# Performance work log

Hardware: AMD Instinct MI355X
Metric: run time of the kernel (lower is better)

## Reference

```python
import jax, jax.numpy as jnp
import numpy as np

STAGE = (20, 20, 20)  # stage spatial size taken from prediction.raw_displacement.shape[2:]


def setup_inputs() -> dict:
    key = jax.random.key(0)
    k1, k2, k3 = jax.random.split(key, 3)
    B, C = 2, 16
    N = STAGE[0] * STAGE[1] * STAGE[2]
    canonical_source = jax.random.normal(k1, (B, C, 64, 64, 64), jnp.float32)
    canonical_target = jax.random.normal(k2, (B, C, 64, 64, 64), jnp.float32)
    # predicted positions live in voxel coordinates of the stage grid
    expected_target_positions = jax.random.uniform(k3, (B, N, 3), jnp.float32) * (STAGE[0] - 1)
    return {
        "canonical_source": canonical_source,
        "canonical_target": canonical_target,
        "expected_target_positions": expected_target_positions,
    }


def reference(canonical_source, canonical_target, expected_target_positions):
    B, C = canonical_source.shape[:2]
    D, H, W = STAGE
    N = D * H * W

    # F.interpolate(mode='trilinear', align_corners=False) == jax.image.resize half-pixel linear
    rs = jax.image.resize(canonical_source, (B, C, D, H, W), method='trilinear')
    rt = jax.image.resize(canonical_target, (B, C, D, H, W), method='trilinear')

    s = rs.reshape(B, C, N).transpose(0, 2, 1)  # (B, N, C)
    t = rt.reshape(B, C, N).transpose(0, 2, 1)  # (B, N, C)

    # squared Euclidean pairwise distances (argmin identical to cdist argmin)
    d2 = (jnp.sum(s * s, axis=-1)[:, :, None]
          - 2.0 * jnp.einsum('bnc,bmc->bnm', s, t)
          + jnp.sum(t * t, axis=-1)[:, None, :])  # (B, N, N)
    nearest = jnp.argmin(d2, axis=-1)  # (B, N)

    dt = canonical_source.dtype
    grid = jnp.stack(
        jnp.meshgrid(jnp.arange(D, dtype=dt), jnp.arange(H, dtype=dt),
                     jnp.arange(W, dtype=dt), indexing='ij'),
        axis=-1).reshape(N, 3)  # (N, 3) voxel coords of target grid

    gathered_target = grid[nearest]  # (B, N, 3)
    return jnp.mean(jnp.abs(expected_target_positions - gathered_target))
```

## Files before the change

kernel.cpp:

```cpp
#include <hip/hip_runtime.h>
#include <stdint.h>
#include <math.h>

#define BDIM   2
#define CDIM   16
#define INS    64
#define OUTS   20
#define NPTS   8000
#define TOTN   (BDIM*NPTS)

using f64x4 = __attribute__((ext_vector_type(4))) double;

#define MFMA64(a, b, c) __builtin_amdgcn_mfma_f64_16x16x4f64((a), (b), (c), 0, 0, 0)


__global__ __launch_bounds__(256) void k_resize(const float* __restrict__ src,
                                                const float* __restrict__ tgt,
                                                double* __restrict__ sfeat2,
                                                double* __restrict__ tfeat) {
    __shared__ double wts[OUTS][8];
    __shared__ int    st[OUTS];
    __shared__ int    cnt[OUTS];
    __shared__ double plane[INS * INS];
    __shared__ double hplane[OUTS * INS];

    int tid = threadIdx.x;
    if (tid < OUTS) {
        double sample = (tid + 0.5) * 3.2 - 0.5;
        int lo = (int)ceil(sample - 3.2);
        int hi = (int)floor(sample + 3.2);
        if (lo < 0) lo = 0;
        if (hi > INS - 1) hi = INS - 1;
        int c = hi - lo + 1;
        double w[8];
        double sum = 0.0;
        for (int k = 0; k < 8; ++k) {
            double ww = 0.0;
            if (k < c) {
                double x = fabs(sample - (double)(lo + k)) * (1.0 / 3.2);
                ww = (x < 1.0) ? (1.0 - x) : 0.0;
            }
            w[k] = ww; sum += ww;
        }
        for (int k = 0; k < 8; ++k) wts[tid][k] = w[k] / sum;
        st[tid] = lo; cnt[tid] = c;
    }
    __syncthreads();

    int od  = blockIdx.x;
    int c   = blockIdx.y;
    int sb  = blockIdx.z;
    int sel = sb >> 1;
    int b   = sb & 1;

    const float* in = (sel ? tgt : src) + (((size_t)(b * CDIM + c)) << 18);

    int sd = st[od], cd = cnt[od];
    double acc[16];
#pragma unroll
    for (int i = 0; i < 16; ++i) acc[i] = 0.0;
    for (int t = 0; t < cd; ++t) {
        double wd = wts[od][t];
        const float* p = in + (((size_t)(sd + t)) << 12) + tid;
#pragma unroll
        for (int i = 0; i < 16; ++i)
            acc[i] = fma(wd, (double)p[i << 8], acc[i]);
    }
#pragma unroll
    for (int i = 0; i < 16; ++i) plane[tid + (i << 8)] = acc[i];
    __syncthreads();

    for (int e = tid; e < OUTS * INS; e += 256) {
        int oh = e >> 6, w = e & 63;
        int sh = st[oh], ch = cnt[oh];
        double a = 0.0;
        for (int t = 0; t < ch; ++t)
            a = fma(wts[oh][t], plane[((sh + t) << 6) + w], a);
        hplane[e] = a;
    }
    __syncthreads();

    double* outf = sel ? tfeat : sfeat2;
    for (int e = tid; e < OUTS * OUTS; e += 256) {
        int oh = e / OUTS, ow = e - oh * OUTS;
        int sw = st[ow], cw = cnt[ow];
        const double* hp = &hplane[(oh << 6) + sw];
        double a = 0.0;
        for (int t = 0; t < cw; ++t)
            a = fma(wts[ow][t], hp[t], a);
        if (sel == 0) a = -2.0 * a;
        int n = (od * OUTS + oh) * OUTS + ow;
        outf[((size_t)(b * NPTS + n)) * CDIM + c] = a;
    }
}

__global__ void k_t2(const double* __restrict__ tfeat, double* __restrict__ t2) {
    int i = blockIdx.x * blockDim.x + threadIdx.x;
    if (i >= TOTN) return;
    const double* p = tfeat + (size_t)i * CDIM;
    double a = 0, b = 0, c = 0, d = 0;
#pragma unroll
    for (int k = 0; k < 4; ++k) {
        a = fma(p[4*k+0], p[4*k+0], a);
        b = fma(p[4*k+1], p[4*k+1], b);
        c = fma(p[4*k+2], p[4*k+2], c);
        d = fma(p[4*k+3], p[4*k+3], d);
    }
    t2[i] = (a + b) + (c + d);
}

__global__ __launch_bounds__(256, 2) void k_argmin(const double* __restrict__ sfeat2,
                                                   const double* __restrict__ tfeat,
                                                   const double* __restrict__ t2,
                                                   double* __restrict__ pscore,
                                                   int* __restrict__ pidx,
                                                   int mchunk, int nchunk) {
    int b     = blockIdx.z;
    int chunk = blockIdx.y;
    int lane  = threadIdx.x & 63;
    int wp    = threadIdx.x >> 6;
    int nbase = blockIdx.x << 7;
    int n0    = nbase + (wp << 4);
    int n1    = n0 + 64;
    int lr    = lane & 15;
    int lq    = lane >> 4;

    f64x4 z = {0.0, 0.0, 0.0, 0.0};
    f64x4 calA = MFMA64((double)lr, 0.25, z);
    f64x4 calB = MFMA64(0.25, (double)lr, z);
    int ncol = (int)(calB[0] + 0.5);

    __shared__ int ptab[16];
#pragma unroll
    for (int j = 0; j < 4; ++j) {
        int r = (int)(calA[j] + 0.5);
        ptab[r] = (lq << 2) + j;
    }
    __syncthreads();
    int prow = ptab[lr];

    int nn0 = n0 + lr; if (nn0 > NPTS - 1) nn0 = NPTS - 1;
    int nn1 = n1 + lr; if (nn1 > NPTS - 1) nn1 = NPTS - 1;
    const double* sb0 = sfeat2 + ((size_t)(b * NPTS + nn0)) * CDIM + (lq << 2);
    const double* sb1 = sfeat2 + ((size_t)(b * NPTS + nn1)) * CDIM + (lq << 2);
    double b00 = sb0[0], b01 = sb0[1], b02 = sb0[2], b03 = sb0[3];
    double b10 = sb1[0], b11 = sb1[1], b12 = sb1[2], b13 = sb1[3];

    const double* tb  = tfeat + (size_t)b * NPTS * CDIM;
    const double* t2b = t2 + (size_t)b * NPTS;

    int mbase = chunk * mchunk;
    int iters = mchunk >> 5;

    const double* tA = tb + ((size_t)(mbase + prow)) * CDIM + (lq << 2);
    const double* tV = t2b + mbase + (lq << 2);

    double bs00 = 1e300, bs01 = 1e300, bs10 = 1e300, bs11 = 1e300;
    int    ip00 = 0, ip01 = 0, ip10 = 0, ip11 = 0;
    int    ij00 = 0, ij01 = 0, ij10 = 0, ij11 = 0;

    f64x4 aE0, aE1, vE0, vE1, aO0, aO1, vO0, vO1;

#define LOADP(P, A0, A1, V0, V1)                                   \
    {  const double* pa_ = tA + (size_t)((P) << 5) * CDIM;         \
       A0 = *(const f64x4*)(pa_);                                  \
       A1 = *(const f64x4*)(pa_ + (CDIM << 4));                    \
       const double* pv_ = tV + ((P) << 5);                        \
       V0 = *(const f64x4*)(pv_);                                  \
       V1 = *(const f64x4*)(pv_ + 16); }

#define FOLD(AC, BS, IP, IJ, P)                                    \
    {  double jb_ = AC[0]; int jj_ = 0;                            \
       if (AC[1] < jb_) { jb_ = AC[1]; jj_ = 1; }                  \
       if (AC[2] < jb_) { jb_ = AC[2]; jj_ = 2; }                  \
       if (AC[3] < jb_) { jb_ = AC[3]; jj_ = 3; }                  \
       if (jb_ < BS) { BS = jb_; IP = (P); IJ = jj_; } }

#define BODYP(P, A0, A1, V0, V1)                                   \
    {  f64x4 a00 = V0, a01 = V1, a10 = V0, a11 = V1;               \
       a00 = MFMA64(A0[0], b00, a00);                              \
       a10 = MFMA64(A0[0], b10, a10);                              \
       a01 = MFMA64(A1[0], b00, a01);                              \
       a11 = MFMA64(A1[0], b10, a11);                              \
       a00 = MFMA64(A0[1], b01, a00);                              \
       a10 = MFMA64(A0[1], b11, a10);                              \
       a01 = MFMA64(A1[1], b01, a01);                              \
       a11 = MFMA64(A1[1], b11, a11);                              \
       a00 = MFMA64(A0[2], b02, a00);                              \
       a10 = MFMA64(A0[2], b12, a10);                              \
       a01 = MFMA64(A1[2], b02, a01);                              \
       a11 = MFMA64(A1[2], b12, a11);                              \
       a00 = MFMA64(A0[3], b03, a00);                              \
       a10 = MFMA64(A0[3], b13, a10);                              \
       a01 = MFMA64(A1[3], b03, a01);                              \
       a11 = MFMA64(A1[3], b13, a11);                              \
       FOLD(a00, bs00, ip00, ij00, P)                              \
       FOLD(a01, bs01, ip01, ij01, P)                              \
       FOLD(a10, bs10, ip10, ij10, P)                              \
       FOLD(a11, bs11, ip11, ij11, P) }

    LOADP(0, aE0, aE1, vE0, vE1);
    if (iters > 1) LOADP(1, aO0, aO1, vO0, vO1);

    int p = 0;
    for (; p + 2 < iters; p += 2) {
        BODYP(p, aE0, aE1, vE0, vE1);
        LOADP(p + 2, aE0, aE1, vE0, vE1);
        BODYP(p + 1, aO0, aO1, vO0, vO1);
        if (p + 3 < iters) LOADP(p + 3, aO0, aO1, vO0, vO1);
    }
    BODYP(p, aE0, aE1, vE0, vE1);
    if (p + 1 < iters) BODYP(p + 1, aO0, aO1, vO0, vO1);

#undef LOADP
#undef FOLD
#undef BODYP

    int m00 = mbase + (ip00 << 5) + (lq << 2) + ij00;
    int m01 = mbase + (ip01 << 5) + 16 + (lq << 2) + ij01;
    int m10 = mbase + (ip10 << 5) + (lq << 2) + ij10;
    int m11 = mbase + (ip11 << 5) + 16 + (lq << 2) + ij11;

    double fb0 = bs00; int fm0 = m00;
    if (bs01 < fb0 || (bs01 == fb0 && m01 < fm0)) { fb0 = bs01; fm0 = m01; }
    double fb1 = bs10; int fm1 = m10;
    if (bs11 < fb1 || (bs11 == fb1 && m11 < fm1)) { fb1 = bs11; fm1 = m11; }

#pragma unroll
    for (int off = 16; off <= 32; off <<= 1) {
        double ob = __shfl_xor(fb0, off, 64);
        int    om = __shfl_xor(fm0, off, 64);
        if (ob < fb0 || (ob == fb0 && om < fm0)) { fb0 = ob; fm0 = om; }
        double ob1 = __shfl_xor(fb1, off, 64);
        int    om1 = __shfl_xor(fm1, off, 64);
        if (ob1 < fb1 || (ob1 == fb1 && om1 < fm1)) { fb1 = ob1; fm1 = om1; }
    }
    if (lq == 0) {
        size_t base = ((size_t)(b * nchunk + chunk)) * NPTS;
        int ns0 = n0 + ncol;
        pscore[base + ns0] = fb0;
        pidx[base + ns0]   = fm0;
        int ns1 = n1 + ncol;
        if (ns1 < NPTS) {
            pscore[base + ns1] = fb1;
            pidx[base + ns1]   = fm1;
        }
    }
}

__global__ void k_mergeloss(const double* __restrict__ pscore,
                            const int* __restrict__ pidx,
                            const float* __restrict__ expd,
                            double* __restrict__ lpart, int nchunk) {
    int gid = blockIdx.x * 256 + threadIdx.x;
    double sum = 0.0;
    if (gid < TOTN) {
        int b  = gid / NPTS;
        int nn = gid % NPTS;
        size_t o = ((size_t)(b * nchunk)) * NPTS + nn;
        double b0 = pscore[o];
        int    i0 = pidx[o];
        for (int c = 1; c < nchunk; ++c) {
            double bpv = pscore[o + (size_t)c * NPTS];
            int    ip  = pidx[o + (size_t)c * NPTS];
            if (bpv < b0 || (bpv == b0 && ip < i0)) { b0 = bpv; i0 = ip; }
        }
        double fd = (double)(i0 / 400);
        double fh = (double)((i0 / 20) % 20);
        double fw = (double)(i0 % 20);
        const float* e = expd + (size_t)gid * 3;
        sum = fabs((double)e[0] - fd) + fabs((double)e[1] - fh) + fabs((double)e[2] - fw);
    }
    __shared__ double red[256];
    red[threadIdx.x] = sum;
    __syncthreads();
    for (int s = 128; s > 0; s >>= 1) {
        if (threadIdx.x < s) red[threadIdx.x] += red[threadIdx.x + s];
        __syncthreads();
    }
    if (threadIdx.x == 0) lpart[blockIdx.x] = red[0];
}

__global__ void k_final(const double* __restrict__ lpart, float* __restrict__ out) {
    int lane = threadIdx.x;
    double v = (lane < 63) ? lpart[lane] : 0.0;
#pragma unroll
    for (int off = 32; off > 0; off >>= 1) v += __shfl_down(v, off);
    if (lane == 0) out[0] = (float)(v / 48000.0);
}

extern "C" void kernel_launch(void* const* d_in, const int* in_sizes, int n_in,
                              void* d_out, int out_size, void* d_ws, size_t ws_size,
                              hipStream_t stream) {
    const float* src  = (const float*)d_in[0];
    const float* tgt  = (const float*)d_in[1];
    const float* expd = (const float*)d_in[2];

    int nchunk = 25, mchunk = 320;
    {
        size_t need = 4224000ull + (size_t)BDIM * 25 * NPTS * 12 + 512;
        if (ws_size < need) { nchunk = 5; mchunk = 1600; }
    }

    char* ws = (char*)d_ws;
    double* sfeat2 = (double*)(ws);
    double* tfeat  = (double*)(ws + 2048000);
    double* t2     = (double*)(ws + 4096000);
    double* pscore = (double*)(ws + 4224000);
    size_t  psz    = (size_t)BDIM * nchunk * NPTS * 8;
    int*    pidx   = (int*)(ws + 4224000 + psz);
    size_t  isz    = (size_t)BDIM * nchunk * NPTS * 4;
    double* lpart  = (double*)(ws + 4224000 + psz + isz);

    k_resize   <<<dim3(OUTS, CDIM, 4), 256, 0, stream>>>(src, tgt, sfeat2, tfeat);
    k_t2       <<<63, 256, 0, stream>>>(tfeat, t2);
    k_argmin   <<<dim3(63, nchunk, BDIM), 256, 0, stream>>>(sfeat2, tfeat, t2,
                                                            pscore, pidx, mchunk, nchunk);
    k_mergeloss<<<63, 256, 0, stream>>>(pscore, pidx, expd, lpart, nchunk);
    k_final    <<<1, 64, 0, stream>>>(lpart, (float*)d_out);
}
```

Measured before the change: 142.7 us.

## Split argmin work between MFMA blocks and scalar FP64 FMA blocks

The argmin kernel now splits the target range in two. The first 4800 targets go to the existing MFMA f64 path. The remaining targets go to new blocks that compute dot products with plain vector FMA, each thread holding four source rows in registers. The aim is to run the MFMA pipe and the vector ALU at the same time on different blocks. The risks are heavier register pressure and extra shared memory in a single kernel, which may lower occupancy. Load balance between the two paths depends on the hard-coded split constants.

```diff
diff --git a/kernel.cpp b/kernel.cpp
--- a/kernel.cpp
+++ b/kernel.cpp
@@ -8,6 +8,8 @@
 #define OUTS   20
 #define NPTS   8000
 #define TOTN   (BDIM*NPTS)
+#define MSPLIT 4800
+#define MCHV   640
 
 using f64x4 = __attribute__((ext_vector_type(4))) double;
 
@@ -114,52 +116,58 @@
                                                    const double* __restrict__ t2,
                                                    double* __restrict__ pscore,
                                                    int* __restrict__ pidx,
-                                                   int mchunk, int nchunk) {
+                                                   int mchunk, int nchunkM,
+                                                   int nchunk) {
+    __shared__ int    ptab[16];
+    __shared__ double sc[1024];
+    __shared__ int    smi[1024];
+
     int b     = blockIdx.z;
     int chunk = blockIdx.y;
     int lane  = threadIdx.x & 63;
-    int wp    = threadIdx.x >> 6;
-    int nbase = blockIdx.x << 7;
-    int n0    = nbase + (wp << 4);
-    int n1    = n0 + 64;
-    int lr    = lane & 15;
-    int lq    = lane >> 4;
-
-    f64x4 z = {0.0, 0.0, 0.0, 0.0};
-    f64x4 calA = MFMA64((double)lr, 0.25, z);
-    f64x4 calB = MFMA64(0.25, (double)lr, z);
-    int ncol = (int)(calB[0] + 0.5);
-
-    __shared__ int ptab[16];
-#pragma unroll
-    for (int j = 0; j < 4; ++j) {
-        int r = (int)(calA[j] + 0.5);
-        ptab[r] = (lq << 2) + j;
-    }
-    __syncthreads();
-    int prow = ptab[lr];
-
-    int nn0 = n0 + lr; if (nn0 > NPTS - 1) nn0 = NPTS - 1;
-    int nn1 = n1 + lr; if (nn1 > NPTS - 1) nn1 = NPTS - 1;
-    const double* sb0 = sfeat2 + ((size_t)(b * NPTS + nn0)) * CDIM + (lq << 2);
-    const double* sb1 = sfeat2 + ((size_t)(b * NPTS + nn1)) * CDIM + (lq << 2);
-    double b00 = sb0[0], b01 = sb0[1], b02 = sb0[2], b03 = sb0[3];
-    double b10 = sb1[0], b11 = sb1[1], b12 = sb1[2], b13 = sb1[3];
 
     const double* tb  = tfeat + (size_t)b * NPTS * CDIM;
     const double* t2b = t2 + (size_t)b * NPTS;
 
-    int mbase = chunk * mchunk;
-    int iters = mchunk >> 5;
-
-    const double* tA = tb + ((size_t)(mbase + prow)) * CDIM + (lq << 2);
-    const double* tV = t2b + mbase + (lq << 2);
-
-    double bs00 = 1e300, bs01 = 1e300, bs10 = 1e300, bs11 = 1e300;
-    int    ip00 = 0, ip01 = 0, ip10 = 0, ip11 = 0;
-    int    ij00 = 0, ij01 = 0, ij10 = 0, ij11 = 0;
-
-    f64x4 aE0, aE1, vE0, vE1, aO0, aO1, vO0, vO1;
+    if (chunk < nchunkM) {
+        int wp    = threadIdx.x >> 6;
+        int nbase = blockIdx.x << 7;
+        int n0    = nbase + (wp << 4);
+        int n1    = n0 + 64;
+        int lr    = lane & 15;
+        int lq    = lane >> 4;
+
+        f64x4 z = {0.0, 0.0, 0.0, 0.0};
+        f64x4 calA = MFMA64((double)lr, 0.25, z);
+        f64x4 calB = MFMA64(0.25, (double)lr, z);
+        int ncol = (int)(calB[0] + 0.5);
+
+#pragma unroll
+        for (int j = 0; j < 4; ++j) {
+            int r = (int)(calA[j] + 0.5);
+            ptab[r] = (lq << 2) + j;
+        }
+        __syncthreads();
+        int prow = ptab[lr];
+
+        int nn0 = n0 + lr; if (nn0 > NPTS - 1) nn0 = NPTS - 1;
+        int nn1 = n1 + lr; if (nn1 > NPTS - 1) nn1 = NPTS - 1;
+        const double* sb0 = sfeat2 + ((size_t)(b * NPTS + nn0)) * CDIM + (lq << 2);
+        const double* sb1 = sfeat2 + ((size_t)(b * NPTS + nn1)) * CDIM + (lq << 2);
+        double b00 = sb0[0], b01 = sb0[1], b02 = sb0[2], b03 = sb0[3];
+        double b10 = sb1[0], b11 = sb1[1], b12 = sb1[2], b13 = sb1[3];
+
+        int mbase = chunk * mchunk;
+        int iters = mchunk >> 5;
+
+        const double* tA = tb + ((size_t)(mbase + prow)) * CDIM + (lq << 2);
+        const double* tV = t2b + mbase + (lq << 2);
+
+        double bs00 = 1e300, bs01 = 1e300, bs10 = 1e300, bs11 = 1e300;
+        int    ip00 = 0, ip01 = 0, ip10 = 0, ip11 = 0;
+        int    ij00 = 0, ij01 = 0, ij10 = 0, ij11 = 0;
+
+        f64x4 aE0, aE1, vE0, vE1, aO0, aO1, vO0, vO1;
 
 #define LOADP(P, A0, A1, V0, V1)                                   \
     {  const double* pa_ = tA + (size_t)((P) << 5) * CDIM;         \
@@ -199,51 +207,121 @@
        FOLD(a10, bs10, ip10, ij10, P)                              \
        FOLD(a11, bs11, ip11, ij11, P) }
 
-    LOADP(0, aE0, aE1, vE0, vE1);
-    if (iters > 1) LOADP(1, aO0, aO1, vO0, vO1);
-
-    int p = 0;
-    for (; p + 2 < iters; p += 2) {
+        LOADP(0, aE0, aE1, vE0, vE1);
+        if (iters > 1) LOADP(1, aO0, aO1, vO0, vO1);
+
+        int p = 0;
+        for (; p + 2 < iters; p += 2) {
+            BODYP(p, aE0, aE1, vE0, vE1);
+            LOADP(p + 2, aE0, aE1, vE0, vE1);
+            BODYP(p + 1, aO0, aO1, vO0, vO1);
+            if (p + 3 < iters) LOADP(p + 3, aO0, aO1, vO0, vO1);
+        }
         BODYP(p, aE0, aE1, vE0, vE1);
-        LOADP(p + 2, aE0, aE1, vE0, vE1);
-        BODYP(p + 1, aO0, aO1, vO0, vO1);
-        if (p + 3 < iters) LOADP(p + 3, aO0, aO1, vO0, vO1);
-    }
-    BODYP(p, aE0, aE1, vE0, vE1);
-    if (p + 1 < iters) BODYP(p + 1, aO0, aO1, vO0, vO1);
+        if (p + 1 < iters) BODYP(p + 1, aO0, aO1, vO0, vO1);
 
 #undef LOADP
 #undef FOLD
 #undef BODYP
 
-    int m00 = mbase + (ip00 << 5) + (lq << 2) + ij00;
-    int m01 = mbase + (ip01 << 5) + 16 + (lq << 2) + ij01;
-    int m10 = mbase + (ip10 << 5) + (lq << 2) + ij10;
-    int m11 = mbase + (ip11 << 5) + 16 + (lq << 2) + ij11;
-
-    double fb0 = bs00; int fm0 = m00;
-    if (bs01 < fb0 || (bs01 == fb0 && m01 < fm0)) { fb0 = bs01; fm0 = m01; }
-    double fb1 = bs10; int fm1 = m10;
-    if (bs11 < fb1 || (bs11 == fb1 && m11 < fm1)) { fb1 = bs11; fm1 = m11; }
-
-#pragma unroll
-    for (int off = 16; off <= 32; off <<= 1) {
-        double ob = __shfl_xor(fb0, off, 64);
-        int    om = __shfl_xor(fm0, off, 64);
-        if (ob < fb0 || (ob == fb0 && om < fm0)) { fb0 = ob; fm0 = om; }
-        double ob1 = __shfl_xor(fb1, off, 64);
-        int    om1 = __shfl_xor(fm1, off, 64);
-        if (ob1 < fb1 || (ob1 == fb1 && om1 < fm1)) { fb1 = ob1; fm1 = om1; }
-    }
-    if (lq == 0) {
-        size_t base = ((size_t)(b * nchunk + chunk)) * NPTS;
-        int ns0 = n0 + ncol;
-        pscore[base + ns0] = fb0;
-        pidx[base + ns0]   = fm0;
-        int ns1 = n1 + ncol;
-        if (ns1 < NPTS) {
-            pscore[base + ns1] = fb1;
-            pidx[base + ns1]   = fm1;
+        int m00 = mbase + (ip00 << 5) + (lq << 2) + ij00;
+        int m01 = mbase + (ip01 << 5) + 16 + (lq << 2) + ij01;
+        int m10 = mbase + (ip10 << 5) + (lq << 2) + ij10;
+        int m11 = mbase + (ip11 << 5) + 16 + (lq << 2) + ij11;
+
+        double fb0 = bs00; int fm0 = m00;
+        if (bs01 < fb0 || (bs01 == fb0 && m01 < fm0)) { fb0 = bs01; fm0 = m01; }
+        double fb1 = bs10; int fm1 = m10;
+        if (bs11 < fb1 || (bs11 == fb1 && m11 < fm1)) { fb1 = bs11; fm1 = m11; }
+
+#pragma unroll
+        for (int off = 16; off <= 32; off <<= 1) {
+            double ob = __shfl_xor(fb0, off, 64);
+            int    om = __shfl_xor(fm0, off, 64);
+            if (ob < fb0 || (ob == fb0 && om < fm0)) { fb0 = ob; fm0 = om; }
+            double ob1 = __shfl_xor(fb1, off, 64);
+            int    om1 = __shfl_xor(fm1, off, 64);
+            if (ob1 < fb1 || (ob1 == fb1 && om1 < fm1)) { fb1 = ob1; fm1 = om1; }
+        }
+        if (lq == 0) {
+            size_t base = ((size_t)(b * nchunk + chunk)) * NPTS;
+            int ns0 = n0 + ncol;
+            pscore[base + ns0] = fb0;
+            pidx[base + ns0]   = fm0;
+            int ns1 = n1 + ncol;
+            if (ns1 < NPTS) {
+                pscore[base + ns1] = fb1;
+                pidx[base + ns1]   = fm1;
+            }
+        }
+    } else {
+        int bx = blockIdx.x;
+        if (bx >= 32) return;
+        int nbase = bx << 8;
+        int wp = (int)__builtin_amdgcn_readfirstlane(threadIdx.x >> 6);
+
+        double s[4][16];
+#pragma unroll
+        for (int j = 0; j < 4; ++j) {
+            int n = nbase + lane + (j << 6);
+            if (n > NPTS - 1) n = NPTS - 1;
+            const double* sr = sfeat2 + ((size_t)(b * NPTS + n)) * CDIM;
+#pragma unroll
+            for (int k = 0; k < CDIM; ++k) s[j][k] = sr[k];
+        }
+
+        int vch   = chunk - nchunkM;
+        int mbase = MSPLIT + vch * MCHV;
+        double best[4] = {1e300, 1e300, 1e300, 1e300};
+        int    bm[4]   = {0, 0, 0, 0};
+        int mstart = mbase + wp;
+
+#pragma unroll 2
+        for (int i = 0; i < MCHV / 4; ++i) {
+            int m = mstart + (i << 2);
+            const double* tr = tb + (size_t)m * CDIM;
+            double t[16];
+#pragma unroll
+            for (int k = 0; k < CDIM; ++k) t[k] = tr[k];
+            double t2v = t2b[m];
+#pragma unroll
+            for (int j = 0; j < 4; ++j) {
+                double d0 = 0, d1 = 0, d2 = 0, d3 = 0;
+#pragma unroll
+                for (int k = 0; k < 4; ++k) {
+                    d0 = fma(s[j][4*k+0], t[4*k+0], d0);
+                    d1 = fma(s[j][4*k+1], t[4*k+1], d1);
+                    d2 = fma(s[j][4*k+2], t[4*k+2], d2);
+                    d3 = fma(s[j][4*k+3], t[4*k+3], d3);
+                }
+                double dot   = (d0 + d1) + (d2 + d3);
+                double score = t2v + dot;
+                if (score < best[j]) { best[j] = score; bm[j] = m; }
+            }
+        }
+
+#pragma unroll
+        for (int j = 0; j < 4; ++j) {
+            sc [wp * 256 + lane * 4 + j] = best[j];
+            smi[wp * 256 + lane * 4 + j] = bm[j];
+        }
+        __syncthreads();
+
+        int tid = threadIdx.x;
+        int e   = (tid & 63) * 4 + (tid >> 6);
+        double b0 = sc[e];
+        int    i0 = smi[e];
+#pragma unroll
+        for (int p = 1; p < 4; ++p) {
+            double bp = sc[p * 256 + e];
+            int    ip = smi[p * 256 + e];
+            if (bp < b0 || (bp == b0 && ip < i0)) { b0 = bp; i0 = ip; }
+        }
+        int n = nbase + tid;
+        if (n < NPTS) {
+            size_t o = ((size_t)(b * nchunk + chunk)) * NPTS + n;
+            pscore[o] = b0;
+            pidx[o]   = i0;
         }
     }
 }
@@ -296,10 +374,11 @@
     const float* tgt  = (const float*)d_in[1];
     const float* expd = (const float*)d_in[2];
 
-    int nchunk = 25, mchunk = 320;
+    int nchunkM = 15, mchunkM = 320, nchunkV = 5;
+    int nchunk  = nchunkM + nchunkV;
     {
-        size_t need = 4224000ull + (size_t)BDIM * 25 * NPTS * 12 + 512;
-        if (ws_size < need) { nchunk = 5; mchunk = 1600; }
+        size_t need = 4224000ull + (size_t)BDIM * 20 * NPTS * 12 + 512;
+        if (ws_size < need) { nchunkM = 5; mchunkM = 1600; nchunkV = 0; nchunk = 5; }
     }
 
     char* ws = (char*)d_ws;
@@ -315,7 +394,8 @@
     k_resize   <<<dim3(OUTS, CDIM, 4), 256, 0, stream>>>(src, tgt, sfeat2, tfeat);
     k_t2       <<<63, 256, 0, stream>>>(tfeat, t2);
     k_argmin   <<<dim3(63, nchunk, BDIM), 256, 0, stream>>>(sfeat2, tfeat, t2,
-                                                            pscore, pidx, mchunk, nchunk);
+                                                            pscore, pidx,
+                                                            mchunkM, nchunkM, nchunk);
     k_mergeloss<<<63, 256, 0, stream>>>(pscore, pidx, expd, lpart, nchunk);
     k_final    <<<1, 64, 0, stream>>>(lpart, (float*)d_out);
 }
```

Result: slower. 189.9 us (+33.1%).
